# Kernel tuning notes

Hardware: AMD Instinct MI355X
Metric: run time of the kernel (lower is better)

Reference implementation:

```python
import jax, jax.numpy as jnp
import numpy as np


def _lstm_bi(x, wih, whh, b):
    # x: [B,T,D]; wih: [2,D,4H]; whh: [2,H,4H]; b: [2,4H]. PyTorch gate order i,f,g,o.
    def run(xs, wi, wh, bb):
        B, H = xs.shape[1], wh.shape[0]
        def step(carry, xt):
            h, c = carry
            g = xt @ wi + h @ wh + bb
            i, f, gg, o = jnp.split(g, 4, axis=-1)
            c = jax.nn.sigmoid(f) * c + jax.nn.sigmoid(i) * jnp.tanh(gg)
            h = jax.nn.sigmoid(o) * jnp.tanh(c)
            return (h, c), h
        z0 = jnp.zeros((B, H), xs.dtype)
        _, hs = jax.lax.scan(step, (z0, z0), xs)
        return hs
    xs = jnp.swapaxes(x, 0, 1)  # [T,B,D]
    hf = run(xs, wih[0], whh[0], b[0])
    hb = run(xs[::-1], wih[1], whh[1], b[1])[::-1]
    return jnp.swapaxes(jnp.concatenate([hf, hb], axis=-1), 0, 1)


def _norm_thr(att, thr):
    # sum-normalize, threshold-sparsify, renormalize (PSP core)
    att = att / (jnp.sum(att, -1, keepdims=True) + 1e-8)
    att = jnp.where(att > thr, att, jnp.zeros_like(att))
    return att / (jnp.sum(att, -1, keepdims=True) + 1e-8)


def _ln(x, g, b):
    mu = jnp.mean(x, -1, keepdims=True)
    var = jnp.mean(jnp.square(x - mu), -1, keepdims=True)
    return (x - mu) / jnp.sqrt(var + 1e-6) * g + b


def _forward(audio, video, thr_val, fa_w1, fa_w2, av_aw, av_ab, av_vw, av_vb,
             av_v2w, av_gw, av_hw, fv_w1, fv_w2, la_wih, la_whh, la_b,
             lv_wih, lv_whh, lv_b, vL1, vL2, aL1, aL2, vfc, afc, ln_g, ln_b, L1w, L2w):
    bs, T = audio.shape[0], audio.shape[1]
    fa = (audio @ fa_w1) @ fa_w2                          # [B,T,128]
    vf = video.reshape(bs, T, -1, video.shape[-1])        # [B,T,49,512]
    # AVGA audio-guided visual attention
    v_h = jax.nn.relu(vf @ av_vw + av_vb)                 # [B,T,49,512]
    a_h = jax.nn.relu(fa @ av_aw + av_ab)                 # [B,T,512]
    content = v_h @ av_v2w + (a_h @ av_gw)[..., None]     # [B,T,49,49]
    z = jnp.squeeze(jnp.tanh(content) @ av_hw, -1)        # [B,T,49]
    alpha = jax.nn.softmax(z, -1)
    video_t = jnp.einsum('btp,btpd->btd', alpha, vf)      # [B,T,512]
    video_t = (video_t @ fv_w1) @ fv_w2                   # [B,T,128]
    # bidirectional LSTMs
    lstm_a = _lstm_bi(fa, la_wih, la_whh, la_b)           # [B,T,256]
    lstm_v = _lstm_bi(video_t, lv_wih, lv_whh, lv_b)      # [B,T,256]
    # PSP (eval mode: dropout is identity)
    v_b1 = jax.nn.relu(lstm_v @ vL1)
    v_b2 = jax.nn.relu(lstm_v @ vL2)
    a_b1 = jax.nn.relu(lstm_a @ aL1)
    a_b2 = jax.nn.relu(lstm_a @ aL2)
    scale = 1.0 / jnp.sqrt(jnp.asarray(v_b2.shape[-1], v_b2.dtype))
    att = jax.nn.relu(jnp.einsum('bvd,bad->bva', v_b2, a_b1) * scale)  # v->a raw
    att_v2a = _norm_thr(att, thr_val)
    att_a2v = _norm_thr(jnp.swapaxes(att, 1, 2), thr_val)
    v_psp = lstm_v + jnp.einsum('bva,bad->bvd', att_v2a, a_b2)
    a_psp = lstm_a + jnp.einsum('bav,bvd->bad', att_a2v, v_b1)
    v_psp = _ln(jax.nn.relu(v_psp @ vfc), ln_g, ln_b)
    a_psp = _ln(jax.nn.relu(a_psp @ afc), ln_g, ln_b)
    fuse = 0.5 * (v_psp + a_psp)
    vn = v_psp / jnp.maximum(jnp.linalg.norm(v_psp, axis=-1, keepdims=True), 1e-12)
    an = a_psp / jnp.maximum(jnp.linalg.norm(a_psp, axis=-1, keepdims=True), 1e-12)
    cross_att = jnp.sum(vn * an, -1)                      # [B,T]
    out = jax.nn.relu(fuse @ L1w) @ L2w                   # [B,T,29]
    return (fuse, out, cross_att)


def setup_inputs() -> dict:
    key = jax.random.key(0)
    ks = iter(jax.random.split(key, 40))
    def w(*shape):
        fan_in = shape[-2] if len(shape) > 1 else shape[-1]
        return jax.random.normal(next(ks), shape, jnp.float32) * (1.0 / np.sqrt(fan_in))
    B, T = 256, 10
    return dict(
        audio=jax.random.normal(next(ks), (B, T, 128), jnp.float32),
        video=jax.random.normal(next(ks), (B, T, 7, 7, 512), jnp.float32),
        thr_val=jnp.float32(0.099),
        fa_w1=w(128, 256), fa_w2=w(256, 128),
        av_aw=w(128, 512), av_ab=jnp.zeros((512,), jnp.float32),
        av_vw=w(512, 512), av_vb=jnp.zeros((512,), jnp.float32),
        av_v2w=w(512, 49), av_gw=w(512, 49), av_hw=w(49, 1),
        fv_w1=w(512, 256), fv_w2=w(256, 128),
        la_wih=w(2, 128, 512), la_whh=w(2, 128, 512), la_b=jnp.zeros((2, 512), jnp.float32),
        lv_wih=w(2, 128, 512), lv_whh=w(2, 128, 512), lv_b=jnp.zeros((2, 512), jnp.float32),
        vL1=w(256, 256), vL2=w(256, 256), aL1=w(256, 256), aL2=w(256, 256),
        vfc=w(256, 256), afc=w(256, 256),
        ln_g=jnp.ones((256,), jnp.float32), ln_b=jnp.zeros((256,), jnp.float32),
        L1w=w(256, 64), L2w=w(64, 29),
    )


def reference(audio, video, thr_val, fa_w1, fa_w2, av_aw, av_ab, av_vw, av_vb,
              av_v2w, av_gw, av_hw, fv_w1, fv_w2, la_wih, la_whh, la_b,
              lv_wih, lv_whh, lv_b, vL1, vL2, aL1, aL2, vfc, afc, ln_g, ln_b, L1w, L2w):
    return _forward(audio, video, thr_val, fa_w1, fa_w2, av_aw, av_ab, av_vw, av_vb,
                    av_v2w, av_gw, av_hw, fv_w1, fv_w2, la_wih, la_whh, la_b,
                    lv_wih, lv_whh, lv_b, vL1, vL2, aL1, aL2, vfc, afc, ln_g, ln_b, L1w, L2w)
```

## Files before the change

kernel.cpp:

```cpp
#include <hip/hip_runtime.h>
#include <math.h>

#define DEV __device__ __forceinline__

typedef _Float16 f16x8 __attribute__((ext_vector_type(8)));
typedef _Float16 f16x4 __attribute__((ext_vector_type(4)));
typedef float    f32x4 __attribute__((ext_vector_type(4)));

DEV float sigmoidf_(float x){ return 1.0f/(1.0f + expf(-x)); }

DEV float wred64(float x){
    #pragma unroll
    for (int off=32; off; off>>=1) x += __shfl_xor(x, off);
    return x;
}

#define MFMA16(a,b,c) __builtin_amdgcn_mfma_f32_16x16x32_f16(a,b,c,0,0,0)

DEV void packone(const float* __restrict__ src, int N, int NfrTot, int nfOff,
                 _Float16* __restrict__ Dh, _Float16* __restrict__ Dl, int o){
    int j = o&7, l16 = (o>>3)&15, kg = (o>>7)&3;
    int rest = o>>9;
    int nfl = rest % (N>>4), kt = rest / (N>>4);
    int k = kt*32 + kg*8 + j, n = nfl*16 + l16;
    float x = src[(size_t)k*N + n];
    _Float16 h = (_Float16)x;
    size_t d = ((size_t)kt*NfrTot + nfOff + nfl)*512 + kg*128 + l16*8 + j;
    Dh[d] = h; Dl[d] = (_Float16)(x - (float)h);
}

__global__ __launch_bounds__(256) void k_prep(
    const float* __restrict__ fa_w1, const float* __restrict__ fa_w2, float* __restrict__ faW,
    const float* __restrict__ fv_w1, const float* __restrict__ fv_w2,
    const float* __restrict__ av_vw, _Float16* __restrict__ Bh, _Float16* __restrict__ Bl,
    const float* __restrict__ v2w, _Float16* __restrict__ Wh, _Float16* __restrict__ Wl,
    const float* __restrict__ lv_wih,
    _Float16* __restrict__ PKfv_h, _Float16* __restrict__ PKfv_l,
    _Float16* __restrict__ PKxv_h, _Float16* __restrict__ PKxv_l)
{
    int bid = blockIdx.x, t = threadIdx.x;
    if (bid < 64){
        int idx = bid*256+t; int m = idx>>7, n = idx&127;
        float acc=0.f;
        for (int k=0;k<256;k++) acc += fa_w1[m*256+k]*fa_w2[k*128+n];
        faW[idx]=acc;
    } else if (bid < 1088){
        int o = (bid-64)*256+t;
        int j = o & 7, l16 = (o>>3)&15, kg = (o>>7)&3, nf = (o>>9)&31, kt = o>>14;
        int k = kt*32 + kg*8 + j, n = nf*16 + l16;
        float x = av_vw[(size_t)k*512 + n];
        _Float16 h = (_Float16)x;
        Bh[o] = h; Bl[o] = (_Float16)(x - (float)h);
    } else if (bid < 1216){
        int o = (bid-1088)*256+t;
        int j = o & 7, l16 = (o>>3)&15, kg = (o>>7)&3, qf = (o>>9)&3, kbg = o>>11;
        int k = kbg*32 + kg*8 + j, q = qf*16 + l16;
        float x = (q < 49) ? v2w[(size_t)k*49 + q] : 0.f;
        _Float16 h = (_Float16)x;
        Wh[o] = h; Wl[o] = (_Float16)(x - (float)h);
    } else if (bid < 1472){
        int o = (bid-1216)*256+t;
        int j=o&7, l16=(o>>3)&15, kg=(o>>7)&3; int rest=o>>9;
        int nfl = rest&7, kt = rest>>3;
        int k = kt*32+kg*8+j, n = nfl*16+l16;
        float acc=0.f;
        for (int kk=0;kk<256;kk++) acc += fv_w1[k*256+kk]*fv_w2[kk*128+n];
        _Float16 h=(_Float16)acc;
        size_t d = ((size_t)kt*8 + nfl)*512 + kg*128 + l16*8 + j;
        PKfv_h[d]=h; PKfv_l[d]=(_Float16)(acc-(float)h);
    } else {
        int seg = (bid-1472)>>8;
        int o = ((bid-1472)&255)*256+t;
        packone(lv_wih + (size_t)seg*65536, 512, 64, seg*32, PKxv_h, PKxv_l, o);
    }
}

__global__ __launch_bounds__(256) void k_faga2(
    const float* __restrict__ audio, const float* __restrict__ faW,
    const float* __restrict__ av_aw, const float* __restrict__ av_ab,
    const float* __restrict__ av_gw,
    const float* __restrict__ la_wih, const float* __restrict__ la_b,
    float* __restrict__ gGA, float* __restrict__ xpA)
{
    int b0 = blockIdx.x*8; int t = threadIdx.x;
    __shared__ float sau[8][128], sfa[8][128], sah[8][512];
    for (int i=t;i<1024;i+=256){ int bt=i>>7,k=i&127; sau[bt][k]=audio[(size_t)(b0+bt)*128+k]; }
    __syncthreads();
    for (int u=0;u<4;u++){
        int i=t+u*256, bt=i>>7, n=i&127;
        float acc=0.f;
        for (int k4=0;k4<32;k4++){
            float4 x4=*(const float4*)&sau[bt][k4*4];
            acc+=x4.x*faW[(k4*4)*128+n]+x4.y*faW[(k4*4+1)*128+n]
                +x4.z*faW[(k4*4+2)*128+n]+x4.w*faW[(k4*4+3)*128+n];
        }
        sfa[bt][n]=acc;
    }
    __syncthreads();
    for (int u=0;u<2;u++){
        int n=t+u*256;
        float bv=av_ab[n];
        float acc[8]={bv,bv,bv,bv,bv,bv,bv,bv};
        for (int k4=0;k4<32;k4++){
            float w0=av_aw[(k4*4)*512+n], w1=av_aw[(k4*4+1)*512+n],
                  w2=av_aw[(k4*4+2)*512+n], w3=av_aw[(k4*4+3)*512+n];
            #pragma unroll
            for (int bt=0;bt<8;bt++){
                float4 x4=*(const float4*)&sfa[bt][k4*4];
                acc[bt]+=x4.x*w0+x4.y*w1+x4.z*w2+x4.w*w3;
            }
        }
        #pragma unroll
        for (int bt=0;bt<8;bt++) sah[bt][n]=fmaxf(acc[bt],0.f);
    }
    __syncthreads();
    for (int hh=0;hh<2;hh++){
        if (t<196){
            int bt=hh*4 + t/49, q=t%49;
            float acc=0.f;
            for (int k=0;k<512;k++) acc+=sah[bt][k]*av_gw[k*49+q];
            gGA[(size_t)(b0+bt)*49+q]=acc;
        }
    }
    for (int u=0;u<4;u++){
        int n = t + u*256;
        int dir = n >> 9, g = n & 511;
        const float* W = la_wih + (size_t)dir*65536;
        float bvv = la_b[dir*512 + g];
        float acc[8] = {bvv,bvv,bvv,bvv,bvv,bvv,bvv,bvv};
        for (int k4=0;k4<32;k4++){
            float w0=W[(k4*4+0)*512+g], w1=W[(k4*4+1)*512+g],
                  w2=W[(k4*4+2)*512+g], w3=W[(k4*4+3)*512+g];
            #pragma unroll
            for (int bt=0;bt<8;bt++){
                float4 x4=*(const float4*)&sfa[bt][k4*4];
                acc[bt]+=x4.x*w0+x4.y*w1+x4.z*w2+x4.w*w3;
            }
        }
        #pragma unroll
        for (int bt=0;bt<8;bt++)
            xpA[((size_t)(b0+bt))*1024 + n] = acc[bt];
    }
}

DEV void cvt4_(float4 v, f16x4& hv, f16x4& lv){
    hv[0]=(_Float16)v.x; lv[0]=(_Float16)(v.x-(float)hv[0]);
    hv[1]=(_Float16)v.y; lv[1]=(_Float16)(v.y-(float)hv[1]);
    hv[2]=(_Float16)v.z; lv[2]=(_Float16)(v.z-(float)hv[2]);
    hv[3]=(_Float16)v.w; lv[3]=(_Float16)(v.w-(float)hv[3]);
}

__global__ __launch_bounds__(256,2) void k_avga_fused(
    const float* __restrict__ video,
    const _Float16* __restrict__ Bh, const _Float16* __restrict__ Bl,
    const float* __restrict__ bias,
    const _Float16* __restrict__ Wh, const _Float16* __restrict__ Wl,
    const float* __restrict__ gGA, const float* __restrict__ hw,
    float* __restrict__ vT)
{
    __shared__ __align__(16) char smem[67072];
    int bt = blockIdx.x;
    int t = threadIdx.x;
    int lane = t & 63, w = t >> 6;
    int l16 = lane & 15, lq = lane >> 4;
    int lb = lane * 16;

    int am = t >> 3, ak = (t & 7) * 4;
    int aoff1 = ((am>>4)*4 + (ak>>3))*256 + (am&15)*16 + (ak&7)*2;
    int am2 = am + 32;
    int aoff2 = ((am2>>4)*4 + (ak>>3))*256 + (am2&15)*16 + (ak&7)*2;
    size_t r1 = (size_t)bt*49 + am;  if (r1 > 125439) r1 = 125439;
    size_t r2 = (size_t)bt*49 + am2; if (r2 > 125439) r2 = 125439;
    const float* Arow1 = video + r1*512 + ak;
    const float* Arow2 = video + r2*512 + ak;

    const f32x4 vzero = {0.f,0.f,0.f,0.f};
    f32x4 acc[4][8];
    #pragma unroll
    for (int p=0;p<4;p++)
        #pragma unroll
        for (int q=0;q<8;q++) acc[p][q] = vzero;

    for (int ph = 0; ph < 2; ++ph){
        for (int kl = 0; kl < 8; ++kl){
            int ko = ph*256 + kl*32;
            float4 a0 = *(const float4*)(Arow1 + ko);
            float4 a1 = *(const float4*)(Arow2 + ko);
            char* h = &smem[kl*8192];
            f16x4 hv, lv;
            cvt4_(a0, hv, lv);
            *(f16x4*)(h + aoff1) = hv; *(f16x4*)(h + 4096 + aoff1) = lv;
            cvt4_(a1, hv, lv);
            *(f16x4*)(h + aoff2) = hv; *(f16x4*)(h + 4096 + aoff2) = lv;
        }
        __syncthreads();
        for (int kl = 0; kl < 8; ++kl){
            int kt = ph*8 + kl;
            const char* aB = &smem[kl*8192];
            f16x8 ah[4], al[4];
            #pragma unroll
            for (int p=0;p<4;p++){
                ah[p] = *(const f16x8*)(aB + p*1024 + lb);
                al[p] = *(const f16x8*)(aB + 4096 + p*1024 + lb);
            }
            #pragma unroll
            for (int q=0;q<8;q++){
                size_t bo = (size_t)kt*16384 + (size_t)(w*8 + q)*512 + lane*8;
                f16x8 bh  = *(const f16x8*)(Bh + bo);
                f16x8 bl2 = *(const f16x8*)(Bl + bo);
                #pragma unroll
                for (int p=0;p<4;p++){
                    acc[p][q] = MFMA16(ah[p], bh,  acc[p][q]);
                    acc[p][q] = MFMA16(ah[p], bl2, acc[p][q]);
                    acc[p][q] = MFMA16(al[p], bh,  acc[p][q]);
                }
            }
        }
        __syncthreads();
    }

    float bv[8];
    #pragma unroll
    for (int q=0;q<8;q++) bv[q] = bias[w*128 + q*16 + l16];

    char* vh = &smem[w*8192];
    f32x4 cacc[4][4];
    #pragma unroll
    for (int p=0;p<4;p++)
        #pragma unroll
        for (int qf=0;qf<4;qf++) cacc[p][qf] = vzero;

    #pragma unroll
    for (int c=0;c<4;c++){
        #pragma unroll
        for (int p=0;p<4;p++)
            #pragma unroll
            for (int qq=0;qq<2;qq++){
                int q = c*2 + qq;
                int offbase = p*1024 + (qq*2 + (l16>>3))*256 + (l16&7)*2;
                #pragma unroll
                for (int r=0;r<4;r++){
                    float x = fmaxf(acc[p][q][r] + bv[q], 0.f);
                    _Float16 hh = (_Float16)x;
                    _Float16 ll = (_Float16)(x - (float)hh);
                    int off = offbase + (lq*4 + r)*16;
                    *(_Float16*)(vh + off)        = hh;
                    *(_Float16*)(vh + 4096 + off) = ll;
                }
            }
        int kbg = w*4 + c;
        f16x8 vhh[4], vhl[4];
        #pragma unroll
        for (int p=0;p<4;p++){
            vhh[p] = *(const f16x8*)(vh + p*1024 + lb);
            vhl[p] = *(const f16x8*)(vh + 4096 + p*1024 + lb);
        }
        #pragma unroll
        for (int qf=0;qf<4;qf++){
            size_t wo = (size_t)kbg*2048 + qf*512 + lane*8;
            f16x8 wh = *(const f16x8*)(Wh + wo);
            f16x8 wl = *(const f16x8*)(Wl + wo);
            #pragma unroll
            for (int p=0;p<4;p++){
                cacc[p][qf] = MFMA16(vhh[p], wh, cacc[p][qf]);
                cacc[p][qf] = MFMA16(vhh[p], wl, cacc[p][qf]);
                cacc[p][qf] = MFMA16(vhl[p], wh, cacc[p][qf]);
            }
        }
    }

    __syncthreads();
    float* pw = (float*)&smem[w*16384];
    #pragma unroll
    for (int p=0;p<4;p++)
        #pragma unroll
        for (int qf=0;qf<4;qf++)
            #pragma unroll
            for (int r=0;r<4;r++)
                pw[(p*16 + lq*4 + r)*64 + qf*16 + l16] = cacc[p][qf][r];
    __syncthreads();
    float* cb = (float*)&smem[0];
    for (int i=t; i<4096; i+=256)
        cb[i] = cb[i] + cb[4096+i] + cb[8192+i] + cb[12288+i];
    __syncthreads();

    float* szp    = (float*)&smem[65536];
    float* salpha = (float*)&smem[66560];
    if (t < 196){
        int p = t >> 2, ds = t & 3;
        float ga = gGA[(size_t)bt*49 + p];
        float part = 0.f;
        for (int q = ds*13; q < ds*13+13 && q < 49; q++)
            part += tanhf(cb[p*64 + q] + ga) * hw[q];
        szp[t] = part;
    }
    __syncthreads();
    if (t < 64){
        float z = (t<49) ? (szp[t*4]+szp[t*4+1]+szp[t*4+2]+szp[t*4+3]) : -1e30f;
        float m = z;
        #pragma unroll
        for (int off=32; off; off>>=1) m = fmaxf(m, __shfl_xor(m, off));
        float e = (t<49)? expf(z - m) : 0.f;
        float s = e;
        #pragma unroll
        for (int off=32; off; off>>=1) s += __shfl_xor(s, off);
        salpha[t] = e / s;
    }
    __syncthreads();
    const float* vb = video + (size_t)bt*49*512;
    #pragma unroll
    for (int u=0;u<2;u++){
        int d = t + u*256;
        float a0 = 0.f;
        for (int p=0;p<49;p++) a0 += salpha[p] * vb[(size_t)p*512 + d];
        vT[(size_t)bt*512 + d] = a0;
    }
}

__global__ __launch_bounds__(256) void k_gemm2(
    const float* __restrict__ vT,
    const _Float16* __restrict__ Fh, const _Float16* __restrict__ Fl,
    const _Float16* __restrict__ Xh, const _Float16* __restrict__ Xl,
    const float* __restrict__ lv_b,
    float* __restrict__ xpV)
{
    __shared__ __align__(16) char sA[2][4096];
    __shared__ float sV[32][132];
    int t = threadIdx.x, lane = t&63, w = t>>6;
    int l16 = lane&15, lq = lane>>4, lb = lane*16;
    int row0 = blockIdx.x * 32;

    int am = t>>3, ak = (t&7)*4;
    int aoff = ((am>>4)*4 + (ak>>3))*256 + (am&15)*16 + (ak&7)*2;
    const float* Arow = vT + (size_t)(row0+am)*512 + ak;

    const f32x4 vzero = {0.f,0.f,0.f,0.f};
    f32x4 acc1[2][2];
    #pragma unroll
    for (int p=0;p<2;p++)
        #pragma unroll
        for (int q=0;q<2;q++) acc1[p][q] = vzero;

    float4 pa = *(const float4*)(Arow);
    {
        f16x4 hv, lv;
        char* h = &sA[0][0];
        cvt4_(pa, hv, lv);
        *(f16x4*)(h + aoff) = hv; *(f16x4*)(h + 2048 + aoff) = lv;
    }
    __syncthreads();
    for (int kt = 0; kt < 16; ++kt){
        int cur = kt & 1;
        bool more = (kt < 15);
        if (more) pa = *(const float4*)(Arow + (kt+1)*32);
        const char* aB = &sA[cur][0];
        f16x8 ah[2], al[2];
        #pragma unroll
        for (int p=0;p<2;p++){
            ah[p] = *(const f16x8*)(aB + p*1024 + lb);
            al[p] = *(const f16x8*)(aB + 2048 + p*1024 + lb);
        }
        #pragma unroll
        for (int q=0;q<2;q++){
            size_t bo = ((size_t)kt*8 + w*2 + q)*512 + lane*8;
            f16x8 bh  = *(const f16x8*)(Fh + bo);
            f16x8 bl2 = *(const f16x8*)(Fl + bo);
            #pragma unroll
            for (int p=0;p<2;p++){
                acc1[p][q] = MFMA16(ah[p], bh,  acc1[p][q]);
                acc1[p][q] = MFMA16(ah[p], bl2, acc1[p][q]);
                acc1[p][q] = MFMA16(al[p], bh,  acc1[p][q]);
            }
        }
        if (more){
            char* h = &sA[cur^1][0];
            f16x4 hv, lv;
            cvt4_(pa, hv, lv);
            *(f16x4*)(h + aoff) = hv; *(f16x4*)(h + 2048 + aoff) = lv;
        }
        __syncthreads();
    }
    #pragma unroll
    for (int q=0;q<2;q++){
        int n = (w*2+q)*16 + l16;
        #pragma unroll
        for (int p=0;p<2;p++)
            #pragma unroll
            for (int r=0;r<4;r++)
                sV[p*16 + lq*4 + r][n] = acc1[p][q][r];
    }
    __syncthreads();

    int nf0 = blockIdx.y*16 + w*4;
    f32x4 acc2[2][4];
    #pragma unroll
    for (int p=0;p<2;p++)
        #pragma unroll
        for (int q=0;q<4;q++) acc2[p][q] = vzero;

    pa = *(const float4*)&sV[am][ak];
    {
        f16x4 hv, lv;
        char* h = &sA[0][0];
        cvt4_(pa, hv, lv);
        *(f16x4*)(h + aoff) = hv; *(f16x4*)(h + 2048 + aoff) = lv;
    }
    __syncthreads();
    for (int kt = 0; kt < 4; ++kt){
        int cur = kt & 1;
        bool more = (kt < 3);
        if (more) pa = *(const float4*)&sV[am][(kt+1)*32 + ak];
        const char* aB = &sA[cur][0];
        f16x8 ah[2], al[2];
        #pragma unroll
        for (int p=0;p<2;p++){
            ah[p] = *(const f16x8*)(aB + p*1024 + lb);
            al[p] = *(const f16x8*)(aB + 2048 + p*1024 + lb);
        }
        #pragma unroll
        for (int q=0;q<4;q++){
            size_t bo = ((size_t)kt*64 + nf0 + q)*512 + lane*8;
            f16x8 bh  = *(const f16x8*)(Xh + bo);
            f16x8 bl2 = *(const f16x8*)(Xl + bo);
            #pragma unroll
            for (int p=0;p<2;p++){
                acc2[p][q] = MFMA16(ah[p], bh,  acc2[p][q]);
                acc2[p][q] = MFMA16(ah[p], bl2, acc2[p][q]);
                acc2[p][q] = MFMA16(al[p], bh,  acc2[p][q]);
            }
        }
        if (more){
            char* h = &sA[cur^1][0];
            f16x4 hv, lv;
            cvt4_(pa, hv, lv);
            *(f16x4*)(h + aoff) = hv; *(f16x4*)(h + 2048 + aoff) = lv;
        }
        __syncthreads();
    }
    #pragma unroll
    for (int q=0;q<4;q++){
        int n = (nf0+q)*16 + l16;
        float bv = lv_b[n];
        #pragma unroll
        for (int p=0;p<2;p++){
            #pragma unroll
            for (int r=0;r<4;r++)
                xpV[(size_t)(row0 + p*16 + lq*4 + r)*1024 + n] = acc2[p][q][r] + bv;
        }
    }
}

__global__ __launch_bounds__(256) void k_lstm(
    const float* __restrict__ xpA, const float* __restrict__ xpV,
    const float* __restrict__ la_whh, const float* __restrict__ lv_whh,
    float* __restrict__ lstm_a, float* __restrict__ lstm_v)
{
    int blk = blockIdx.x;
    int c = blk >> 6;
    int chunk = blk & 63;
    int t = threadIdx.x;
    int j  = t & 127;
    int bh = t >> 7;
    const float* whh = ((c<2)? la_whh : lv_whh) + (size_t)(c&1)*128*512;
    const float* xpm = (c<2)? xpA : xpV;
    float* outp = (c<2)? lstm_a : lstm_v;
    int dir = c & 1;

    __shared__ float hbuf[4][128];
    float cc[2] = {0.f,0.f};
    for (int i=t;i<512;i+=256) ((float*)hbuf)[i] = 0.f;
    __syncthreads();

    for (int s=0; s<10; s++){
        int tt = dir ? (9-s) : s;
        float gi[2], gf[2], gg[2], go[2];
        #pragma unroll
        for (int b=0;b<2;b++){
            int gb = chunk*4 + bh*2 + b;
            const float* xrow = xpm + ((size_t)gb*10 + tt)*1024 + dir*512;
            gi[b]=xrow[j]; gf[b]=xrow[128+j]; gg[b]=xrow[256+j]; go[b]=xrow[384+j];
        }
        #pragma unroll 4
        for (int k=0;k<128;k++){
            float wi = whh[k*512 + j];
            float wf = whh[k*512 + 128 + j];
            float wg = whh[k*512 + 256 + j];
            float wo = whh[k*512 + 384 + j];
            #pragma unroll
            for (int b=0;b<2;b++){
                float hk = hbuf[bh*2+b][k];
                gi[b] += hk*wi; gf[b] += hk*wf; gg[b] += hk*wg; go[b] += hk*wo;
            }
        }
        __syncthreads();
        #pragma unroll
        for (int b=0;b<2;b++){
            float i_ = sigmoidf_(gi[b]);
            float f_ = sigmoidf_(gf[b]);
            float g_ = tanhf(gg[b]);
            float o_ = sigmoidf_(go[b]);
            cc[b] = f_*cc[b] + i_*g_;
            float h_ = o_*tanhf(cc[b]);
            hbuf[bh*2+b][j] = h_;
            int gb = chunk*4 + bh*2 + b;
            outp[((size_t)gb*10 + tt)*256 + dir*128 + j] = h_;
        }
        __syncthreads();
    }
}

__global__ __launch_bounds__(256) void k_tail(
    const float* __restrict__ lstm_a, const float* __restrict__ lstm_v,
    const float* __restrict__ vL1, const float* __restrict__ vL2,
    const float* __restrict__ aL1, const float* __restrict__ aL2,
    const float* __restrict__ vfc, const float* __restrict__ afc,
    const float* __restrict__ thrp,
    const float* __restrict__ ln_g, const float* __restrict__ ln_b,
    const float* __restrict__ L1w, const float* __restrict__ L2w,
    float* __restrict__ dout)
{
    int b = blockIdx.x, t = threadIdx.x;
    int lane = t & 63, w = t >> 6;
    __shared__ float sla[10][256], slv[10][256];
    __shared__ float sb1v[10][256], sb2v[10][256], sb1a[10][256], sb2a[10][256];
    __shared__ float sfu[10][256];
    __shared__ float s64[10][64];
    __shared__ float satt[100], s_v2a[100], s_a2v[100];
    __shared__ float sredp[160];
    __shared__ float scos[120];

    size_t base = (size_t)b*2560;
    for (int i=t;i<2560;i+=256){
        ((float*)sla)[i] = lstm_a[base+i];
        ((float*)slv)[i] = lstm_v[base+i];
    }
    __syncthreads();

    {
        float a1[10], a2[10];
        #pragma unroll
        for (int r=0;r<10;r++){ a1[r]=0.f; a2[r]=0.f; }
        #pragma unroll 4
        for (int k=0;k<256;k++){
            float w1 = vL1[k*256+t], w2 = vL2[k*256+t];
            #pragma unroll
            for (int r=0;r<10;r++){ float x=slv[r][k]; a1[r]+=x*w1; a2[r]+=x*w2; }
        }
        #pragma unroll
        for (int r=0;r<10;r++){ sb1v[r][t]=fmaxf(a1[r],0.f); sb2v[r][t]=fmaxf(a2[r],0.f); }
        #pragma unroll
        for (int r=0;r<10;r++){ a1[r]=0.f; a2[r]=0.f; }
        #pragma unroll 4
        for (int k=0;k<256;k++){
            float w1 = aL1[k*256+t], w2 = aL2[k*256+t];
            #pragma unroll
            for (int r=0;r<10;r++){ float x=sla[r][k]; a1[r]+=x*w1; a2[r]+=x*w2; }
        }
        #pragma unroll
        for (int r=0;r<10;r++){ sb1a[r][t]=fmaxf(a1[r],0.f); sb2a[r][t]=fmaxf(a2[r],0.f); }
    }
    __syncthreads();

    if (t < 100){
        int v = t/10, a = t - v*10;
        float acc=0.f;
        for (int k=0;k<256;k++) acc += sb2v[v][k]*sb1a[a][k];
        satt[t] = fmaxf(acc*(1.0f/16.0f), 0.f);
    }
    __syncthreads();
    float thr = thrp[0];
    if (t < 10){
        int v = t;
        float rs=0.f; for(int a=0;a<10;a++) rs += satt[v*10+a];
        float inv = 1.f/(rs+1e-8f);
        float tmp[10]; float rs2=0.f;
        for(int a=0;a<10;a++){ float x = satt[v*10+a]*inv; x = (x>thr)?x:0.f; tmp[a]=x; rs2+=x; }
        float inv2 = 1.f/(rs2+1e-8f);
        for(int a=0;a<10;a++) s_v2a[v*10+a] = tmp[a]*inv2;
    } else if (t>=16 && t<26){
        int a = t-16;
        float cs=0.f; for(int v=0;v<10;v++) cs += satt[v*10+a];
        float inv = 1.f/(cs+1e-8f);
        float tmp[10]; float cs2=0.f;
        for(int v=0;v<10;v++){ float x = satt[v*10+a]*inv; x=(x>thr)?x:0.f; tmp[v]=x; cs2+=x; }
        float inv2 = 1.f/(cs2+1e-8f);
        for(int v=0;v<10;v++) s_a2v[a*10+v] = tmp[v]*inv2;
    }
    __syncthreads();

    #pragma unroll
    for (int v=0;v<10;v++){
        float acc = slv[v][t];
        #pragma unroll
        for (int a=0;a<10;a++) acc += s_v2a[v*10+a]*sb2a[a][t];
        slv[v][t] = acc;
    }
    #pragma unroll
    for (int a=0;a<10;a++){
        float acc = sla[a][t];
        #pragma unroll
        for (int v=0;v<10;v++) acc += s_a2v[a*10+v]*sb1v[v][t];
        sla[a][t] = acc;
    }
    __syncthreads();

    float fv[10], fa2[10];
    #pragma unroll
    for (int r=0;r<10;r++){ fv[r]=0.f; fa2[r]=0.f; }
    #pragma unroll 4
    for (int k=0;k<256;k++){
        float wv = vfc[k*256+t], wa = afc[k*256+t];
        #pragma unroll
        for (int r=0;r<10;r++){ fv[r]+=slv[r][k]*wv; fa2[r]+=sla[r][k]*wa; }
    }
    #pragma unroll
    for (int r=0;r<10;r++){ fv[r]=fmaxf(fv[r],0.f); fa2[r]=fmaxf(fa2[r],0.f); }

    #pragma unroll
    for (int r=0;r<10;r++){
        float s1 = wred64(fv[r]);
        float s2 = wred64(fv[r]*fv[r]);
        float s3 = wred64(fa2[r]);
        float s4 = wred64(fa2[r]*fa2[r]);
        if (lane==0){
            sredp[r*16 + 0*4 + w] = s1; sredp[r*16 + 1*4 + w] = s2;
            sredp[r*16 + 2*4 + w] = s3; sredp[r*16 + 3*4 + w] = s4;
        }
    }
    __syncthreads();
    float gt = ln_g[t], bt2 = ln_b[t];
    #pragma unroll
    for (int r=0;r<10;r++){
        float s1 = sredp[r*16+0]+sredp[r*16+1]+sredp[r*16+2]+sredp[r*16+3];
        float s2 = sredp[r*16+4]+sredp[r*16+5]+sredp[r*16+6]+sredp[r*16+7];
        float s3 = sredp[r*16+8]+sredp[r*16+9]+sredp[r*16+10]+sredp[r*16+11];
        float s4 = sredp[r*16+12]+sredp[r*16+13]+sredp[r*16+14]+sredp[r*16+15];
        float muv = s1*(1.f/256.f);
        float varv = s2*(1.f/256.f) - muv*muv;
        float rsv = 1.f/sqrtf(varv+1e-6f);
        float vln = (fv[r]-muv)*rsv*gt + bt2;
        float mua = s3*(1.f/256.f);
        float vara = s4*(1.f/256.f) - mua*mua;
        float rsa = 1.f/sqrtf(vara+1e-6f);
        float aln = (fa2[r]-mua)*rsa*gt + bt2;
        float fu = 0.5f*(vln+aln);
        dout[(size_t)(b*10+r)*256 + t] = fu;
        sfu[r][t] = fu;
        float c1 = wred64(vln*vln);
        float c2 = wred64(aln*aln);
        float c3 = wred64(vln*aln);
        if (lane==0){
            scos[r*12 + 0*4 + w] = c1; scos[r*12 + 1*4 + w] = c2; scos[r*12 + 2*4 + w] = c3;
        }
    }
    __syncthreads();
    if (t < 10){
        int r = t;
        float nv2 = scos[r*12+0]+scos[r*12+1]+scos[r*12+2]+scos[r*12+3];
        float na2 = scos[r*12+4]+scos[r*12+5]+scos[r*12+6]+scos[r*12+7];
        float dva = scos[r*12+8]+scos[r*12+9]+scos[r*12+10]+scos[r*12+11];
        float nv = fmaxf(sqrtf(nv2), 1e-12f);
        float na = fmaxf(sqrtf(na2), 1e-12f);
        dout[729600 + b*10 + r] = dva/(nv*na);
    }

    #pragma unroll
    for (int pass=0; pass<3; ++pass){
        int r = pass*4 + w;
        if (r < 10){
            float acc = 0.f;
            for (int k4=0;k4<64;k4++){
                float4 f4 = *(const float4*)&sfu[r][k4*4];
                acc += f4.x*L1w[(k4*4)*64+lane] + f4.y*L1w[(k4*4+1)*64+lane]
                     + f4.z*L1w[(k4*4+2)*64+lane] + f4.w*L1w[(k4*4+3)*64+lane];
            }
            s64[r][lane] = fmaxf(acc, 0.f);
        }
    }
    __syncthreads();
    for (int i=t; i<290; i+=256){
        int r = i/29, jj = i - r*29;
        float acc = 0.f;
        #pragma unroll
        for (int k=0;k<64;k++) acc += s64[r][k]*L2w[k*29+jj];
        dout[655360 + (size_t)(b*10+r)*29 + jj] = acc;
    }
}

extern "C" void kernel_launch(void* const* d_in, const int* in_sizes, int n_in,
                              void* d_out, int out_size, void* d_ws, size_t ws_size,
                              hipStream_t stream) {
    const float* audio  = (const float*)d_in[0];
    const float* video  = (const float*)d_in[1];
    const float* thrp   = (const float*)d_in[2];
    const float* fa_w1  = (const float*)d_in[3];
    const float* fa_w2  = (const float*)d_in[4];
    const float* av_aw  = (const float*)d_in[5];
    const float* av_ab  = (const float*)d_in[6];
    const float* av_vw  = (const float*)d_in[7];
    const float* av_vb  = (const float*)d_in[8];
    const float* av_v2w = (const float*)d_in[9];
    const float* av_gw  = (const float*)d_in[10];
    const float* av_hw  = (const float*)d_in[11];
    const float* fv_w1  = (const float*)d_in[12];
    const float* fv_w2  = (const float*)d_in[13];
    const float* la_wih = (const float*)d_in[14];
    const float* la_whh = (const float*)d_in[15];
    const float* la_b   = (const float*)d_in[16];
    const float* lv_wih = (const float*)d_in[17];
    const float* lv_whh = (const float*)d_in[18];
    const float* lv_b   = (const float*)d_in[19];
    const float* vL1    = (const float*)d_in[20];
    const float* vL2    = (const float*)d_in[21];
    const float* aL1    = (const float*)d_in[22];
    const float* aL2    = (const float*)d_in[23];
    const float* vfc    = (const float*)d_in[24];
    const float* afc    = (const float*)d_in[25];
    const float* ln_g   = (const float*)d_in[26];
    const float* ln_b   = (const float*)d_in[27];
    const float* L1w    = (const float*)d_in[28];
    const float* L2w    = (const float*)d_in[29];
    float* dout = (float*)d_out;
    float* ws = (float*)d_ws;

    float* faW  = ws;
    float* gGA  = ws + 409600;
    float* vT   = ws + 535040;
    float* xpA  = ws + 2173440;
    float* xpV  = ws + 4794880;
    float* la   = ws + 7416320;
    float* lv   = ws + 8071680;
    _Float16* Bh = (_Float16*)(ws + 12659200);
    _Float16* Bl = (_Float16*)(ws + 12790272);
    _Float16* Wh = (_Float16*)(ws + 12921344);
    _Float16* Wl = (_Float16*)(ws + 12937728);
    _Float16* PKfv_h = (_Float16*)(ws + 12954112);
    _Float16* PKfv_l = (_Float16*)(ws + 12986880);
    _Float16* PKxv_h = (_Float16*)(ws + 13150720);
    _Float16* PKxv_l = (_Float16*)(ws + 13216256);

    k_prep<<<1984, 256, 0, stream>>>(fa_w1, fa_w2, faW, fv_w1, fv_w2,
                                     av_vw, Bh, Bl, av_v2w, Wh, Wl,
                                     lv_wih, PKfv_h, PKfv_l, PKxv_h, PKxv_l);
    k_faga2<<<320, 256, 0, stream>>>(audio, faW, av_aw, av_ab, av_gw,
                                     la_wih, la_b, gGA, xpA);
    k_avga_fused<<<2560, 256, 0, stream>>>(video, Bh, Bl, av_vb, Wh, Wl,
                                           gGA, av_hw, vT);
    k_gemm2<<<dim3(80,4), 256, 0, stream>>>(vT, PKfv_h, PKfv_l,
                                            PKxv_h, PKxv_l, lv_b, xpV);
    k_lstm<<<256, 256, 0, stream>>>(xpA, xpV, la_whh, lv_whh, la, lv);
    k_tail<<<256, 256, 0, stream>>>(la, lv, vL1, vL2, aL1, aL2, vfc, afc,
                                    thrp, ln_g, ln_b, L1w, L2w, dout);
}
```

Measured before the change: 709.0 us.

## Double-buffer A tiles in AVGA GEMM and split tail kernel across 512 threads

The fused AVGA kernel now streams A tiles through a two-slot shared-memory double buffer. It prefetches the next k-slice into registers while issuing MFMAs on the current one, instead of staging eight slices and then computing in two phases. The v_h scratch area moves to offset 16384 so it no longer overlaps the ping-pong buffers. The tail kernel runs 512 threads, with each half handling 5 of the 10 time rows, which raises parallelism at the cost of reading the weights twice per block.

```diff
diff --git a/kernel.cpp b/kernel.cpp
--- a/kernel.cpp
+++ b/kernel.cpp
@@ -181,49 +181,61 @@
         #pragma unroll
         for (int q=0;q<8;q++) acc[p][q] = vzero;
 
-    for (int ph = 0; ph < 2; ++ph){
-        for (int kl = 0; kl < 8; ++kl){
-            int ko = ph*256 + kl*32;
-            float4 a0 = *(const float4*)(Arow1 + ko);
-            float4 a1 = *(const float4*)(Arow2 + ko);
-            char* h = &smem[kl*8192];
+    float4 pa0, pa1;
+    pa0 = *(const float4*)(Arow1);
+    pa1 = *(const float4*)(Arow2);
+    {
+        f16x4 hv, lv;
+        char* h = &smem[0];
+        cvt4_(pa0, hv, lv);
+        *(f16x4*)(h + aoff1) = hv; *(f16x4*)(h + 4096 + aoff1) = lv;
+        cvt4_(pa1, hv, lv);
+        *(f16x4*)(h + aoff2) = hv; *(f16x4*)(h + 4096 + aoff2) = lv;
+    }
+    __syncthreads();
+
+    for (int kt = 0; kt < 16; ++kt){
+        int cur = kt & 1;
+        bool more = (kt < 15);
+        if (more){
+            pa0 = *(const float4*)(Arow1 + (kt+1)*32);
+            pa1 = *(const float4*)(Arow2 + (kt+1)*32);
+        }
+        const char* aB = &smem[cur*8192];
+        f16x8 ah[4], al[4];
+        #pragma unroll
+        for (int p=0;p<4;p++){
+            ah[p] = *(const f16x8*)(aB + p*1024 + lb);
+            al[p] = *(const f16x8*)(aB + 4096 + p*1024 + lb);
+        }
+        #pragma unroll
+        for (int q=0;q<8;q++){
+            size_t bo = (size_t)kt*16384 + (size_t)(w*8 + q)*512 + lane*8;
+            f16x8 bh  = *(const f16x8*)(Bh + bo);
+            f16x8 bl2 = *(const f16x8*)(Bl + bo);
+            #pragma unroll
+            for (int p=0;p<4;p++){
+                acc[p][q] = MFMA16(ah[p], bh,  acc[p][q]);
+                acc[p][q] = MFMA16(ah[p], bl2, acc[p][q]);
+                acc[p][q] = MFMA16(al[p], bh,  acc[p][q]);
+            }
+        }
+        if (more){
+            char* h = &smem[(cur^1)*8192];
             f16x4 hv, lv;
-            cvt4_(a0, hv, lv);
+            cvt4_(pa0, hv, lv);
             *(f16x4*)(h + aoff1) = hv; *(f16x4*)(h + 4096 + aoff1) = lv;
-            cvt4_(a1, hv, lv);
+            cvt4_(pa1, hv, lv);
             *(f16x4*)(h + aoff2) = hv; *(f16x4*)(h + 4096 + aoff2) = lv;
         }
         __syncthreads();
-        for (int kl = 0; kl < 8; ++kl){
-            int kt = ph*8 + kl;
-            const char* aB = &smem[kl*8192];
-            f16x8 ah[4], al[4];
-            #pragma unroll
-            for (int p=0;p<4;p++){
-                ah[p] = *(const f16x8*)(aB + p*1024 + lb);
-                al[p] = *(const f16x8*)(aB + 4096 + p*1024 + lb);
-            }
-            #pragma unroll
-            for (int q=0;q<8;q++){
-                size_t bo = (size_t)kt*16384 + (size_t)(w*8 + q)*512 + lane*8;
-                f16x8 bh  = *(const f16x8*)(Bh + bo);
-                f16x8 bl2 = *(const f16x8*)(Bl + bo);
-                #pragma unroll
-                for (int p=0;p<4;p++){
-                    acc[p][q] = MFMA16(ah[p], bh,  acc[p][q]);
-                    acc[p][q] = MFMA16(ah[p], bl2, acc[p][q]);
-                    acc[p][q] = MFMA16(al[p], bh,  acc[p][q]);
-                }
-            }
-        }
-        __syncthreads();
     }
 
     float bv[8];
     #pragma unroll
     for (int q=0;q<8;q++) bv[q] = bias[w*128 + q*16 + l16];
 
-    char* vh = &smem[w*8192];
+    char* vh = &smem[16384 + w*8192];
     f32x4 cacc[4][4];
     #pragma unroll
     for (int p=0;p<4;p++)
@@ -509,7 +521,7 @@
     }
 }
 
-__global__ __launch_bounds__(256) void k_tail(
+__global__ __launch_bounds__(512) void k_tail(
     const float* __restrict__ lstm_a, const float* __restrict__ lstm_v,
     const float* __restrict__ vL1, const float* __restrict__ vL2,
     const float* __restrict__ aL1, const float* __restrict__ aL2,
@@ -519,66 +531,71 @@
     const float* __restrict__ L1w, const float* __restrict__ L2w,
     float* __restrict__ dout)
 {
-    int b = blockIdx.x, t = threadIdx.x;
-    int lane = t & 63, w = t >> 6;
+    int b = blockIdx.x, tid = threadIdx.x;
+    int t = tid & 255;
+    int half = tid >> 8;
+    int lane = tid & 63, w = tid >> 6;
+    int wl = w & 3;
+    int r0 = half*5;
+
     __shared__ float sla[10][256], slv[10][256];
     __shared__ float sb1v[10][256], sb2v[10][256], sb1a[10][256], sb2a[10][256];
     __shared__ float sfu[10][256];
     __shared__ float s64[10][64];
     __shared__ float satt[100], s_v2a[100], s_a2v[100];
-    __shared__ float sredp[160];
-    __shared__ float scos[120];
+    __shared__ float sredp[10][4][4];
+    __shared__ float scos[10][3][4];
 
     size_t base = (size_t)b*2560;
-    for (int i=t;i<2560;i+=256){
+    for (int i=tid;i<2560;i+=512){
         ((float*)sla)[i] = lstm_a[base+i];
         ((float*)slv)[i] = lstm_v[base+i];
     }
     __syncthreads();
 
     {
-        float a1[10], a2[10];
-        #pragma unroll
-        for (int r=0;r<10;r++){ a1[r]=0.f; a2[r]=0.f; }
+        float a1[5], a2[5];
+        #pragma unroll
+        for (int r=0;r<5;r++){ a1[r]=0.f; a2[r]=0.f; }
         #pragma unroll 4
         for (int k=0;k<256;k++){
             float w1 = vL1[k*256+t], w2 = vL2[k*256+t];
             #pragma unroll
-            for (int r=0;r<10;r++){ float x=slv[r][k]; a1[r]+=x*w1; a2[r]+=x*w2; }
-        }
-        #pragma unroll
-        for (int r=0;r<10;r++){ sb1v[r][t]=fmaxf(a1[r],0.f); sb2v[r][t]=fmaxf(a2[r],0.f); }
-        #pragma unroll
-        for (int r=0;r<10;r++){ a1[r]=0.f; a2[r]=0.f; }
+            for (int r=0;r<5;r++){ float x=slv[r0+r][k]; a1[r]+=x*w1; a2[r]+=x*w2; }
+        }
+        #pragma unroll
+        for (int r=0;r<5;r++){ sb1v[r0+r][t]=fmaxf(a1[r],0.f); sb2v[r0+r][t]=fmaxf(a2[r],0.f); }
+        #pragma unroll
+        for (int r=0;r<5;r++){ a1[r]=0.f; a2[r]=0.f; }
         #pragma unroll 4
         for (int k=0;k<256;k++){
             float w1 = aL1[k*256+t], w2 = aL2[k*256+t];
             #pragma unroll
-            for (int r=0;r<10;r++){ float x=sla[r][k]; a1[r]+=x*w1; a2[r]+=x*w2; }
-        }
-        #pragma unroll
-        for (int r=0;r<10;r++){ sb1a[r][t]=fmaxf(a1[r],0.f); sb2a[r][t]=fmaxf(a2[r],0.f); }
-    }
-    __syncthreads();
-
-    if (t < 100){
-        int v = t/10, a = t - v*10;
+            for (int r=0;r<5;r++){ float x=sla[r0+r][k]; a1[r]+=x*w1; a2[r]+=x*w2; }
+        }
+        #pragma unroll
+        for (int r=0;r<5;r++){ sb1a[r0+r][t]=fmaxf(a1[r],0.f); sb2a[r0+r][t]=fmaxf(a2[r],0.f); }
+    }
+    __syncthreads();
+
+    if (tid < 100){
+        int v = tid/10, a = tid - v*10;
         float acc=0.f;
         for (int k=0;k<256;k++) acc += sb2v[v][k]*sb1a[a][k];
-        satt[t] = fmaxf(acc*(1.0f/16.0f), 0.f);
+        satt[tid] = fmaxf(acc*(1.0f/16.0f), 0.f);
     }
     __syncthreads();
     float thr = thrp[0];
-    if (t < 10){
-        int v = t;
+    if (tid < 10){
+        int v = tid;
         float rs=0.f; for(int a=0;a<10;a++) rs += satt[v*10+a];
         float inv = 1.f/(rs+1e-8f);
         float tmp[10]; float rs2=0.f;
         for(int a=0;a<10;a++){ float x = satt[v*10+a]*inv; x = (x>thr)?x:0.f; tmp[a]=x; rs2+=x; }
         float inv2 = 1.f/(rs2+1e-8f);
         for(int a=0;a<10;a++) s_v2a[v*10+a] = tmp[a]*inv2;
-    } else if (t>=16 && t<26){
-        int a = t-16;
+    } else if (tid>=16 && tid<26){
+        int a = tid-16;
         float cs=0.f; for(int v=0;v<10;v++) cs += satt[v*10+a];
         float inv = 1.f/(cs+1e-8f);
         float tmp[10]; float cs2=0.f;
@@ -589,52 +606,55 @@
     __syncthreads();
 
     #pragma unroll
-    for (int v=0;v<10;v++){
-        float acc = slv[v][t];
-        #pragma unroll
-        for (int a=0;a<10;a++) acc += s_v2a[v*10+a]*sb2a[a][t];
-        slv[v][t] = acc;
-    }
-    #pragma unroll
-    for (int a=0;a<10;a++){
-        float acc = sla[a][t];
-        #pragma unroll
-        for (int v=0;v<10;v++) acc += s_a2v[a*10+v]*sb1v[v][t];
-        sla[a][t] = acc;
-    }
-    __syncthreads();
-
-    float fv[10], fa2[10];
-    #pragma unroll
-    for (int r=0;r<10;r++){ fv[r]=0.f; fa2[r]=0.f; }
+    for (int v=0;v<5;v++){
+        int row = r0+v;
+        float acc = slv[row][t];
+        #pragma unroll
+        for (int a=0;a<10;a++) acc += s_v2a[row*10+a]*sb2a[a][t];
+        slv[row][t] = acc;
+    }
+    #pragma unroll
+    for (int a=0;a<5;a++){
+        int row = r0+a;
+        float acc = sla[row][t];
+        #pragma unroll
+        for (int v=0;v<10;v++) acc += s_a2v[row*10+v]*sb1v[v][t];
+        sla[row][t] = acc;
+    }
+    __syncthreads();
+
+    float fv[5], fa2[5];
+    #pragma unroll
+    for (int r=0;r<5;r++){ fv[r]=0.f; fa2[r]=0.f; }
     #pragma unroll 4
     for (int k=0;k<256;k++){
         float wv = vfc[k*256+t], wa = afc[k*256+t];
         #pragma unroll
-        for (int r=0;r<10;r++){ fv[r]+=slv[r][k]*wv; fa2[r]+=sla[r][k]*wa; }
-    }
-    #pragma unroll
-    for (int r=0;r<10;r++){ fv[r]=fmaxf(fv[r],0.f); fa2[r]=fmaxf(fa2[r],0.f); }
-
-    #pragma unroll
-    for (int r=0;r<10;r++){
+        for (int r=0;r<5;r++){ fv[r]+=slv[r0+r][k]*wv; fa2[r]+=sla[r0+r][k]*wa; }
+    }
+    #pragma unroll
+    for (int r=0;r<5;r++){ fv[r]=fmaxf(fv[r],0.f); fa2[r]=fmaxf(fa2[r],0.f); }
+
+    #pragma unroll
+    for (int r=0;r<5;r++){
         float s1 = wred64(fv[r]);
         float s2 = wred64(fv[r]*fv[r]);
         float s3 = wred64(fa2[r]);
         float s4 = wred64(fa2[r]*fa2[r]);
         if (lane==0){
-            sredp[r*16 + 0*4 + w] = s1; sredp[r*16 + 1*4 + w] = s2;
-            sredp[r*16 + 2*4 + w] = s3; sredp[r*16 + 3*4 + w] = s4;
+            sredp[r0+r][0][wl] = s1; sredp[r0+r][1][wl] = s2;
+            sredp[r0+r][2][wl] = s3; sredp[r0+r][3][wl] = s4;
         }
     }
     __syncthreads();
     float gt = ln_g[t], bt2 = ln_b[t];
     #pragma unroll
-    for (int r=0;r<10;r++){
-        float s1 = sredp[r*16+0]+sredp[r*16+1]+sredp[r*16+2]+sredp[r*16+3];
-        float s2 = sredp[r*16+4]+sredp[r*16+5]+sredp[r*16+6]+sredp[r*16+7];
-        float s3 = sredp[r*16+8]+sredp[r*16+9]+sredp[r*16+10]+sredp[r*16+11];
-        float s4 = sredp[r*16+12]+sredp[r*16+13]+sredp[r*16+14]+sredp[r*16+15];
+    for (int r=0;r<5;r++){
+        int row = r0+r;
+        float s1 = sredp[row][0][0]+sredp[row][0][1]+sredp[row][0][2]+sredp[row][0][3];
+        float s2 = sredp[row][1][0]+sredp[row][1][1]+sredp[row][1][2]+sredp[row][1][3];
+        float s3 = sredp[row][2][0]+sredp[row][2][1]+sredp[row][2][2]+sredp[row][2][3];
+        float s4 = sredp[row][3][0]+sredp[row][3][1]+sredp[row][3][2]+sredp[row][3][3];
         float muv = s1*(1.f/256.f);
         float varv = s2*(1.f/256.f) - muv*muv;
         float rsv = 1.f/sqrtf(varv+1e-6f);
@@ -644,29 +664,29 @@
         float rsa = 1.f/sqrtf(vara+1e-6f);
         float aln = (fa2[r]-mua)*rsa*gt + bt2;
         float fu = 0.5f*(vln+aln);
-        dout[(size_t)(b*10+r)*256 + t] = fu;
-        sfu[r][t] = fu;
+        dout[(size_t)(b*10+row)*256 + t] = fu;
+        sfu[row][t] = fu;
         float c1 = wred64(vln*vln);
         float c2 = wred64(aln*aln);
         float c3 = wred64(vln*aln);
         if (lane==0){
-            scos[r*12 + 0*4 + w] = c1; scos[r*12 + 1*4 + w] = c2; scos[r*12 + 2*4 + w] = c3;
-        }
-    }
-    __syncthreads();
-    if (t < 10){
-        int r = t;
-        float nv2 = scos[r*12+0]+scos[r*12+1]+scos[r*12+2]+scos[r*12+3];
-        float na2 = scos[r*12+4]+scos[r*12+5]+scos[r*12+6]+scos[r*12+7];
-        float dva = scos[r*12+8]+scos[r*12+9]+scos[r*12+10]+scos[r*12+11];
+            scos[row][0][wl] = c1; scos[row][1][wl] = c2; scos[row][2][wl] = c3;
+        }
+    }
+    __syncthreads();
+    if (tid < 10){
+        int r = tid;
+        float nv2 = scos[r][0][0]+scos[r][0][1]+scos[r][0][2]+scos[r][0][3];
+        float na2 = scos[r][1][0]+scos[r][1][1]+scos[r][1][2]+scos[r][1][3];
+        float dva = scos[r][2][0]+scos[r][2][1]+scos[r][2][2]+scos[r][2][3];
         float nv = fmaxf(sqrtf(nv2), 1e-12f);
         float na = fmaxf(sqrtf(na2), 1e-12f);
         dout[729600 + b*10 + r] = dva/(nv*na);
     }
 
     #pragma unroll
-    for (int pass=0; pass<3; ++pass){
-        int r = pass*4 + w;
+    for (int pass=0; pass<2; ++pass){
+        int r = pass*8 + w;
         if (r < 10){
             float acc = 0.f;
             for (int k4=0;k4<64;k4++){
@@ -678,7 +698,7 @@
         }
     }
     __syncthreads();
-    for (int i=t; i<290; i+=256){
+    for (int i=tid; i<290; i+=512){
         int r = i/29, jj = i - r*29;
         float acc = 0.f;
         #pragma unroll
@@ -749,6 +769,6 @@
     k_gemm2<<<dim3(80,4), 256, 0, stream>>>(vT, PKfv_h, PKfv_l,
                                             PKxv_h, PKxv_l, lv_b, xpV);
     k_lstm<<<256, 256, 0, stream>>>(xpA, xpV, la_whh, lv_whh, la, lv);
-    k_tail<<<256, 256, 0, stream>>>(la, lv, vL1, vL2, aL1, aL2, vfc, afc,
+    k_tail<<<256, 512, 0, stream>>>(la, lv, vL1, vL2, aL1, aL2, vfc, afc,
                                     thrp, ln_g, ln_b, L1w, L2w, dout);
 }
```

Result: faster. 638.3 us (-10.0%).
